# Optimization experiments

Measured on AMD Instinct MI355X. Metric: run time of the kernel, lower is better.

Reference implementation:

```python
import jax, jax.numpy as jnp
import numpy as np

B, S, V, E, H, NL, DFF = 16, 16, 64, 64, 8, 4, 2048
L = S * V
DH = E // H
NUM_GRIDS = 100
POI_DIM = 8
OV_DIM = 8


def setup_inputs() -> dict:
    key = jax.random.key(0)
    ks = jax.random.split(key, 32)
    sc = 0.05
    inp = {}
    inp['features'] = jax.random.normal(ks[0], (B, S, V, 3), jnp.float32)
    inp['overlap_tag'] = jax.random.randint(ks[1], (B, S, V), 0, 3)
    inp['poi_id'] = jax.random.randint(ks[2], (B, S, V), 0, NUM_GRIDS + 1)
    # embedders
    inp['W_raw'] = jax.random.normal(ks[3], (3, E), jnp.float32) * sc
    inp['b_raw'] = jnp.zeros((E,), jnp.float32)
    inp['pos_tab'] = jax.random.normal(ks[4], (S, E), jnp.float32) * sc
    inp['type_tab'] = jax.random.normal(ks[5], (V, E), jnp.float32) * sc
    inp['poi_tab'] = jax.random.normal(ks[6], (NUM_GRIDS + 1, POI_DIM), jnp.float32) * sc
    inp['overlap_tab'] = jax.random.normal(ks[7], (3, OV_DIM), jnp.float32) * sc
    inp['W_comb'] = jax.random.normal(ks[8], (E + OV_DIM + POI_DIM, E), jnp.float32) * sc
    inp['b_comb'] = jnp.zeros((E,), jnp.float32)
    # transformer layers (stacked over NL)
    inp['Wqkv'] = jax.random.normal(ks[9], (NL, E, 3 * E), jnp.float32) * sc
    inp['bqkv'] = jnp.zeros((NL, 3 * E), jnp.float32)
    inp['Wo'] = jax.random.normal(ks[10], (NL, E, E), jnp.float32) * sc
    inp['bo'] = jnp.zeros((NL, E), jnp.float32)
    inp['ln1_s'] = jnp.ones((NL, E), jnp.float32)
    inp['ln1_b'] = jnp.zeros((NL, E), jnp.float32)
    inp['W1'] = jax.random.normal(ks[11], (NL, E, DFF), jnp.float32) * sc
    inp['b1'] = jnp.zeros((NL, DFF), jnp.float32)
    inp['W2'] = jax.random.normal(ks[12], (NL, DFF, E), jnp.float32) * sc
    inp['b2'] = jnp.zeros((NL, E), jnp.float32)
    inp['ln2_s'] = jnp.ones((NL, E), jnp.float32)
    inp['ln2_b'] = jnp.zeros((NL, E), jnp.float32)
    inp['W_head'] = jax.random.normal(ks[13], (E, 3), jnp.float32) * sc
    inp['b_head'] = jnp.zeros((3,), jnp.float32)
    return inp


def _layer_norm(x, s, b):
    m = x.mean(-1, keepdims=True)
    v = ((x - m) ** 2).mean(-1, keepdims=True)
    return (x - m) / jnp.sqrt(v + 1e-5) * s + b


def _forward(features, overlap_tag, poi_id, W_raw, b_raw, pos_tab, type_tab,
             poi_tab, overlap_tab, W_comb, b_comb, Wqkv, bqkv, Wo, bo,
             ln1_s, ln1_b, W1, b1, W2, b2, ln2_s, ln2_b, W_head, b_head):
    # padding_idx=0 rows are zero (as in nn.Embedding(padding_idx=0))
    poi_tab = poi_tab.at[0].set(0.0)
    overlap_tab = overlap_tab.at[0].set(0.0)

    zero_mask = (features.sum(-1) == 0).reshape(B, L)  # [B, L]
    ov_idx = jnp.maximum(overlap_tag, 0)
    poi_idx = jnp.maximum(poi_id, 0)

    feat_e = features @ W_raw + b_raw                    # [B,S,V,E]
    concat = jnp.concatenate([feat_e, overlap_tab[ov_idx], poi_tab[poi_idx]], axis=-1)
    x = (concat @ W_comb + b_comb).reshape(B, L, E)      # [B,L,E]

    t_idx = jnp.repeat(jnp.arange(S), V)                 # [L]
    v_idx = jnp.tile(jnp.arange(V), S)                   # [L]
    struct_mask = (t_idx[:, None] != t_idx[None, :]) & (v_idx[:, None] != v_idx[None, :])
    full_mask = struct_mask[None] | zero_mask[:, None, :] | zero_mask[:, :, None]  # [B,L,L]
    bias = jnp.where(full_mask, -jnp.inf, 0.0)[:, None, :, :]  # [B,1,L,L]

    x = x + pos_tab[t_idx][None] + type_tab[v_idx][None]

    scale = 1.0 / jnp.sqrt(jnp.asarray(DH, x.dtype))
    for l in range(NL):
        qkv = x @ Wqkv[l] + bqkv[l]                      # [B,L,3E]
        q, k, v = jnp.split(qkv, 3, axis=-1)
        q = q.reshape(B, L, H, DH)
        k = k.reshape(B, L, H, DH)
        v = v.reshape(B, L, H, DH)
        scores = jnp.einsum('bqhd,bkhd->bhqk', q, k) * scale + bias
        attn = jax.nn.softmax(scores, axis=-1)
        o = jnp.einsum('bhqk,bkhd->bqhd', attn, v).reshape(B, L, E)
        x = _layer_norm(x + o @ Wo[l] + bo[l], ln1_s[l], ln1_b[l])
        ff = jax.nn.relu(x @ W1[l] + b1[l]) @ W2[l] + b2[l]
        x = _layer_norm(x + ff, ln2_s[l], ln2_b[l])

    last = x.reshape(B, S, V, E)[:, -1]                  # [B,V,E]
    return last @ W_head + b_head                        # [B,V,3]


def reference(features, overlap_tag, poi_id, W_raw, b_raw, pos_tab, type_tab,
              poi_tab, overlap_tab, W_comb, b_comb, Wqkv, bqkv, Wo, bo,
              ln1_s, ln1_b, W1, b1, W2, b2, ln2_s, ln2_b, W_head, b_head):
    return _forward(features, overlap_tag, poi_id, W_raw, b_raw, pos_tab, type_tab,
                    poi_tab, overlap_tab, W_comb, b_comb, Wqkv, bqkv, Wo, bo,
                    ln1_s, ln1_b, W1, b1, W2, b2, ln2_s, ln2_b, W_head, b_head)
```

## Files before the change

kernel.cpp:

```cpp
#include <hip/hip_runtime.h>
#include <math.h>

#define BB 16
#define SS 16
#define VVV 64
#define EE 64
#define HHH 8
#define NLAYER 4
#define DFF_ 2048
#define LL 1024
#define BL 16384
#define PERL 131072

typedef __attribute__((ext_vector_type(8))) _Float16 half8;
typedef __attribute__((ext_vector_type(4))) _Float16 half4v;
typedef __attribute__((ext_vector_type(2))) _Float16 half2v;
typedef __attribute__((ext_vector_type(4))) float f32x4;

#if defined(__has_builtin)
#if __has_builtin(__builtin_amdgcn_fdot2)
#define HAVE_FDOT2 1
#endif
#endif

#define SW64(m, k)  (((m) << 6) + ((((k) >> 3) ^ ((m) & 7)) << 3) + ((k) & 7))


__global__ __launch_bounds__(256) void k_prep(
    const float* __restrict__ W1, const float* __restrict__ W2,
    const float* __restrict__ Wqkv, const float* __restrict__ Wo,
    const float* __restrict__ Wcomb,
    _Float16* __restrict__ w1f, _Float16* __restrict__ w2f,
    _Float16* __restrict__ wqkvf, _Float16* __restrict__ wof,
    _Float16* __restrict__ wcombt)
{
  __shared__ float t[64 * 65];
  int bx = blockIdx.x;
  int cc = threadIdx.x & 63, rr = threadIdx.x >> 6;

  if (bx >= 272) {
    int r0 = (bx - 272) * 64;
#pragma unroll
    for (int i = 0; i < 16; i++) {
      int r = i * 4 + rr;
      if (r0 + r < 80) t[r * 65 + cc] = Wcomb[(size_t)(r0 + r) * 64 + cc];
    }
    __syncthreads();
#pragma unroll
    for (int i = 0; i < 16; i++) {
      int c = i * 4 + rr;
      if (r0 + c < 80) wcombt[(size_t)cc * 80 + r0 + c] = (_Float16)t[c * 65 + cc];
    }
    return;
  }

  const float* src; _Float16* dst; int astr;
  if (bx < 128) {
    int l = bx >> 5, g = bx & 31;
    src = W1 + (size_t)l * PERL + g * 64; astr = 2048;
    dst = w1f + (size_t)(l * 32 + g) * 4096;
  } else if (bx < 256) {
    int j = bx - 128; int l = j >> 5, g = j & 31;
    src = W2 + (size_t)l * PERL + (size_t)g * 64 * 64; astr = 64;
    dst = w2f + (size_t)(l * 32 + g) * 4096;
  } else if (bx < 268) {
    int j = bx - 256; int l = j / 3, g = j % 3;
    src = Wqkv + (size_t)l * 64 * 192 + g * 64; astr = 192;
    dst = wqkvf + (size_t)(l * 3 + g) * 4096;
  } else {
    int l = bx - 268;
    src = Wo + (size_t)l * 4096; astr = 64;
    dst = wof + (size_t)l * 4096;
  }
#pragma unroll
  for (int i = 0; i < 16; i++) {
    int a = i * 4 + rr;
    t[cc * 65 + a] = src[(size_t)a * astr + cc];
  }
  __syncthreads();
#pragma unroll
  for (int it = 0; it < 2; it++) {
    int c = threadIdx.x + it * 256;
    int frag = c >> 6, lane = c & 63;
    int m = (frag >> 1) * 16 + (lane & 15);
    int k0 = (frag & 1) * 32 + (lane >> 4) * 8;
    const float* tr = &t[m * 65 + k0];
    half8 h;
#pragma unroll
    for (int j = 0; j < 8; j++) h[j] = (_Float16)tr[j];
    *(half8*)&dst[(size_t)c * 8] = h;
  }
}

__device__ __forceinline__ void qkv_nb(
    const half8 (&af)[2][2], const _Float16* __restrict__ wqkvf,
    const float* __restrict__ bqkv, _Float16* __restrict__ qbuf,
    _Float16* __restrict__ kbuf, _Float16* __restrict__ vbuf,
    int bx, int nb, int wm, int wn, int lane)
{
  int quad = lane >> 4, l15 = lane & 15;
  const _Float16* bt = wqkvf + (size_t)nb * 4096;
  half8 bf[2][2];
#pragma unroll
  for (int nt = 0; nt < 2; nt++)
#pragma unroll
    for (int ks = 0; ks < 2; ks++)
      bf[nt][ks] = *(const half8*)&bt[(size_t)(((wn * 2 + nt) * 2 + ks) * 512) +
                                      lane * 8];
  f32x4 acc[2][2];
#pragma unroll
  for (int mt = 0; mt < 2; mt++)
#pragma unroll
    for (int nt = 0; nt < 2; nt++) {
      float bv = bqkv[nb * 64 + wn * 32 + nt * 16 + l15];
      acc[mt][nt] = (f32x4){bv, bv, bv, bv};
    }
#pragma unroll
  for (int ks = 0; ks < 2; ks++)
#pragma unroll
    for (int mt = 0; mt < 2; mt++)
#pragma unroll
      for (int nt = 0; nt < 2; nt++)
        acc[mt][nt] = __builtin_amdgcn_mfma_f32_16x16x32_f16(
            af[mt][ks], bf[nt][ks], acc[mt][nt], 0, 0, 0);
  _Float16* dst = (nb == 0) ? qbuf : ((nb == 1) ? kbuf : vbuf);
#pragma unroll
  for (int mt = 0; mt < 2; mt++)
#pragma unroll
    for (int nt = 0; nt < 2; nt++) {
      int col = wn * 32 + nt * 16 + l15;
      int h = col >> 3, d = col & 7;
#pragma unroll
      for (int r = 0; r < 4; r++) {
        int row = bx * 64 + wm * 32 + mt * 16 + quad * 4 + r;
        int b = row >> 10, rb = row & 1023;
        dst[((size_t)(b * 8 + h) * 1024 + rb) * 8 + d] = (_Float16)acc[mt][nt][r];
      }
    }
}

__global__ __launch_bounds__(256) void k_embqkv(
    const float* __restrict__ features, const int* __restrict__ ovtag,
    const int* __restrict__ poiid, const float* __restrict__ W_raw,
    const float* __restrict__ b_raw, const float* __restrict__ ov_tab,
    const float* __restrict__ poi_tab, const _Float16* __restrict__ wcombt,
    const float* __restrict__ b_comb, const float* __restrict__ pos_tab,
    const float* __restrict__ type_tab, float* __restrict__ x1,
    float* __restrict__ zm, const _Float16* __restrict__ wqkvf,
    const float* __restrict__ bqkv, _Float16* __restrict__ qbuf,
    _Float16* __restrict__ kbuf, _Float16* __restrict__ vbuf)
{
  constexpr int KP = 104;
  __shared__ _Float16 As[64 * KP];
  __shared__ _Float16 Bs[64 * KP];
  __shared__ _Float16 xs[4096];
  int tid = threadIdx.x;
  int raw = blockIdx.x;
  int bx = ((raw & 7) * 2 + ((raw >> 3) >> 4)) * 16 + ((raw >> 3) & 15);
  int m0 = bx * 64;
  int wave = tid >> 6, lane = tid & 63, quad = lane >> 4, l15 = lane & 15;
  int wm = wave >> 1, wn = wave & 1;
  for (int p = tid; p < 1536; p += 256) {
    int r = p / 24, s = p - r * 24; int c = s * 4;
    int row = m0 + r;
    float f0 = features[row * 3 + 0];
    float f1 = features[row * 3 + 1];
    float f2 = features[row * 3 + 2];
    if (s == 0) zm[row] = ((f0 + f1 + f2) == 0.f) ? 1.f : 0.f;
    half4v h;
#pragma unroll
    for (int j = 0; j < 4; j++) {
      int cc = c + j; float v;
      if (cc < 64) {
        v = b_raw[cc] + f0 * W_raw[cc] + f1 * W_raw[64 + cc] + f2 * W_raw[128 + cc];
      } else if (cc < 72) {
        int tt = ovtag[row]; v = (tt <= 0) ? 0.f : ov_tab[tt * 8 + cc - 64];
      } else if (cc < 80) {
        int tt = poiid[row]; v = (tt <= 0) ? 0.f : poi_tab[tt * 8 + cc - 72];
      } else v = 0.f;
      h[j] = (_Float16)v;
    }
    *(half4v*)&As[r * KP + c] = h;
  }
  for (int p = tid; p < 1536; p += 256) {
    int r = p / 24, s = p - r * 24; int c = s * 4;
    half4v h = (half4v){0, 0, 0, 0};
    if (c < 80) h = *(const half4v*)&wcombt[r * 80 + c];
    *(half4v*)&Bs[r * KP + c] = h;
  }
  __syncthreads();
  f32x4 acc[2][2];
#pragma unroll
  for (int mt = 0; mt < 2; mt++)
#pragma unroll
    for (int nt = 0; nt < 2; nt++) {
      float bv = b_comb[wn * 32 + nt * 16 + l15];
      acc[mt][nt] = (f32x4){bv, bv, bv, bv};
    }
#pragma unroll
  for (int ks = 0; ks < 3; ks++) {
    half8 af[2], bf[2];
#pragma unroll
    for (int mt = 0; mt < 2; mt++)
      af[mt] = *(const half8*)&As[(wm * 32 + mt * 16 + l15) * KP + ks * 32 + quad * 8];
#pragma unroll
    for (int nt = 0; nt < 2; nt++)
      bf[nt] = *(const half8*)&Bs[(wn * 32 + nt * 16 + l15) * KP + ks * 32 + quad * 8];
#pragma unroll
    for (int mt = 0; mt < 2; mt++)
#pragma unroll
      for (int nt = 0; nt < 2; nt++)
        acc[mt][nt] = __builtin_amdgcn_mfma_f32_16x16x32_f16(af[mt], bf[nt],
                                                             acc[mt][nt], 0, 0, 0);
  }
#pragma unroll
  for (int mt = 0; mt < 2; mt++)
#pragma unroll
    for (int nt = 0; nt < 2; nt++)
#pragma unroll
      for (int r = 0; r < 4; r++) {
        int lrow = wm * 32 + mt * 16 + quad * 4 + r;
        int row = m0 + lrow;
        int col = wn * 32 + nt * 16 + l15;
        int l = row & (LL - 1);
        float v = acc[mt][nt][r] +
            pos_tab[(l >> 6) * 64 + col] + type_tab[(l & 63) * 64 + col];
        x1[(size_t)row * 64 + col] = v;
        xs[SW64(lrow, col)] = (_Float16)v;
      }
  __syncthreads();
  half8 af[2][2];
#pragma unroll
  for (int mt = 0; mt < 2; mt++)
#pragma unroll
    for (int ks = 0; ks < 2; ks++)
      af[mt][ks] = *(const half8*)&xs[SW64(wm * 32 + mt * 16 + l15,
                                           ks * 32 + quad * 8)];
  for (int nb = 0; nb < 3; nb++)
    qkv_nb(af, wqkvf, bqkv, qbuf, kbuf, vbuf, bx, nb, wm, wn, lane);
}

__global__ __launch_bounds__(256, 4) void k_layer16(
    const _Float16* __restrict__ qin, const _Float16* __restrict__ kin,
    const _Float16* __restrict__ vin, const float* __restrict__ zm,
    const _Float16* __restrict__ wof, const float* __restrict__ bo,
    float* __restrict__ x1,
    const float* __restrict__ ln1_s, const float* __restrict__ ln1_b,
    const _Float16* __restrict__ w1f, const _Float16* __restrict__ w2f,
    const float* __restrict__ b1, const float* __restrict__ b2,
    const float* __restrict__ ln2_s, const float* __restrict__ ln2_b,
    const _Float16* __restrict__ wqkvf, const float* __restrict__ bqkv,
    _Float16* __restrict__ qout, _Float16* __restrict__ kout,
    _Float16* __restrict__ vout, int doqkv,
    const float* __restrict__ Wh, const float* __restrict__ bh,
    float* __restrict__ out)
{
  __shared__ float ots[16 * 68];
  __shared__ float ots2[16 * 68];
  __shared__ __align__(16) _Float16 xs[1024];
  __shared__ float x2f[1024];
  __shared__ __align__(16) _Float16 hs[4][1024];
  __shared__ __align__(16) _Float16 os[1024];
  __shared__ float zsh[1024];
  __shared__ __align__(16) _Float16 qkvt[16 * 200];
  int tid = threadIdx.x;
  int raw = blockIdx.x;
  int bx = ((raw & 7) * 2 + ((raw >> 3) >> 6)) * 64 + ((raw >> 3) & 63);
  int r0 = bx * 16;
  int rb0 = r0 & 1023;
  int b = r0 >> 10;
  int wave = tid >> 6, lane = tid & 63;
  int quad = lane >> 4, l15 = lane & 15;

  for (int p = tid; p < 1024; p += 256)
    zsh[p] = (zm[b * LL + p] != 0.f) ? -20000.f : 0.f;

  half8 obf[2];
#pragma unroll
  for (int ks = 0; ks < 2; ks++)
    obf[ks] = *(const half8*)&wof[(size_t)((wave * 2 + ks) * 512) + lane * 8];
  float x1pre[4];
#pragma unroll
  for (int i = 0; i < 4; i++)
    x1pre[i] = x1[(size_t)(r0 + wave * 4 + i) * 64 + lane];
  float ln1sv = ln1_s[lane], ln1bv = ln1_b[lane];
  float ln2sv = ln2_s[lane], ln2bv = ln2_b[lane];
  float fb2 = b2[lane];
  float bov = bo[wave * 16 + l15];
  __syncthreads();

  {
    int pr = tid >> 1, ksl = tid & 1;
    int lr = pr & 15, hh = pr >> 4;
    int rb = rb0 + lr;
    int tq = rb0 >> 6;
    int vq = rb & 63;
    const _Float16* kb = kin + (size_t)(b * 8 + hh) * 8192;
    const _Float16* vb = vin + (size_t)(b * 8 + hh) * 8192;
    half8 qh = *(const half8*)&qin[(size_t)(b * 8 + hh) * 8192 + (size_t)rb * 8];
    const float scale = 0.3535533905932738f;
    float m = -10000.f, lsum = 0.f;
    float acc[8] = {0.f, 0.f, 0.f, 0.f, 0.f, 0.f, 0.f, 0.f};
    bool zmq = (zsh[rb] < -1.f);

    auto attend = [&](int k) {
      half8 kk = *(const half8*)&kb[(size_t)k * 8];
      half8 vv = *(const half8*)&vb[(size_t)k * 8];
      float s = 0.f;
#ifdef HAVE_FDOT2
#pragma unroll
      for (int j = 0; j < 4; j++) {
        half2v qa = (half2v){qh[2 * j], qh[2 * j + 1]};
        half2v ka = (half2v){kk[2 * j], kk[2 * j + 1]};
        s = __builtin_amdgcn_fdot2(qa, ka, s, false);
      }
#else
#pragma unroll
      for (int j = 0; j < 8; j++) s += (float)qh[j] * (float)kk[j];
#endif
      s = s * scale + zsh[k];
      float nm = fmaxf(m, s);
      float r = __expf(m - nm);
      float p = __expf(s - nm);
      lsum = lsum * r + p;
#pragma unroll
      for (int d = 0; d < 8; d++) acc[d] = acc[d] * r + p * (float)vv[d];
      m = nm;
    };

    if (!zmq) {
#pragma unroll 4
      for (int i = 0; i < 32; i++) attend(tq * 64 + 2 * i + ksl);
      int c = 0;
      for (int tt = 0; tt < 16; tt++) {
        if (tt == tq) continue;
        if ((c & 1) == ksl) attend(tt * 64 + vq);
        c++;
      }
    }
    float m2 = __shfl_xor(m, 1), l2 = __shfl_xor(lsum, 1);
    float nm = fmaxf(m, m2);
    float f1 = __expf(m - nm), f2 = __expf(m2 - nm);
    lsum = lsum * f1 + l2 * f2;
#pragma unroll
    for (int d = 0; d < 8; d++) {
      float a2 = __shfl_xor(acc[d], 1);
      acc[d] = acc[d] * f1 + a2 * f2;
    }
    float inv = (lsum > 0.f) ? 1.f / lsum : 0.f;
    if (ksl == 0) {
      half8 o;
#pragma unroll
      for (int d = 0; d < 8; d++) o[d] = (_Float16)(acc[d] * inv);
      *(half8*)&os[SW64(lr, hh * 8)] = o;
    }
  }
  __syncthreads();

  {
    half8 af[2];
#pragma unroll
    for (int ks = 0; ks < 2; ks++)
      af[ks] = *(const half8*)&os[SW64(l15, ks * 32 + quad * 8)];
    f32x4 acc = (f32x4){bov, bov, bov, bov};
#pragma unroll
    for (int ks = 0; ks < 2; ks++)
      acc = __builtin_amdgcn_mfma_f32_16x16x32_f16(af[ks], obf[ks], acc, 0, 0, 0);
#pragma unroll
    for (int r = 0; r < 4; r++)
      ots[(quad * 4 + r) * 68 + wave * 16 + l15] = acc[r];
  }
  __syncthreads();
  for (int i = 0; i < 4; i++) {
    int row = wave * 4 + i;
    float val = ots[row * 68 + lane] + x1pre[i];
    float sum = val;
#pragma unroll
    for (int o = 32; o > 0; o >>= 1) sum += __shfl_xor(sum, o);
    float mean = sum * (1.f / 64.f);
    float d = val - mean;
    float sq = d * d;
#pragma unroll
    for (int o = 32; o > 0; o >>= 1) sq += __shfl_xor(sq, o);
    float xv = d * rsqrtf(sq * (1.f / 64.f) + 1e-5f) * ln1sv + ln1bv;
    x2f[row * 64 + lane] = xv;
    xs[SW64(row, lane)] = (_Float16)xv;
  }
  __syncthreads();

  half8 xb[2];
#pragma unroll
  for (int ks = 0; ks < 2; ks++)
    xb[ks] = *(const half8*)&xs[SW64(l15, ks * 32 + quad * 8)];
  f32x4 facc[4];
#pragma unroll
  for (int nt = 0; nt < 4; nt++) facc[nt] = (f32x4){0.f, 0.f, 0.f, 0.f};
  _Float16* hw = &hs[wave][0];
  for (int ii = 0; ii < 8; ii++) {
    int g = ii * 4 + wave;
    const _Float16* w1t = w1f + (size_t)g * 4096;
    const _Float16* w2t = w2f + (size_t)g * 4096;
    half8 a1[4][2], b2w[4][2];
#pragma unroll
    for (int t = 0; t < 4; t++)
#pragma unroll
      for (int ks = 0; ks < 2; ks++) {
        a1[t][ks] = *(const half8*)&w1t[(size_t)((t * 2 + ks) * 512) + lane * 8];
        b2w[t][ks] = *(const half8*)&w2t[(size_t)((t * 2 + ks) * 512) + lane * 8];
      }
    f32x4 hacc[4];
#pragma unroll
    for (int ht = 0; ht < 4; ht++) hacc[ht] = (f32x4){0.f, 0.f, 0.f, 0.f};
#pragma unroll
    for (int ks = 0; ks < 2; ks++)
#pragma unroll
      for (int ht = 0; ht < 4; ht++)
        hacc[ht] = __builtin_amdgcn_mfma_f32_16x16x32_f16(a1[ht][ks], xb[ks],
                                                          hacc[ht], 0, 0, 0);
#pragma unroll
    for (int ht = 0; ht < 4; ht++) {
      float4 bb = *(const float4*)&b1[g * 64 + ht * 16 + quad * 4];
      f32x4 hv = hacc[ht];
      half4v hp = (half4v){
          (_Float16)fmaxf(hv[0] + bb.x, 0.f), (_Float16)fmaxf(hv[1] + bb.y, 0.f),
          (_Float16)fmaxf(hv[2] + bb.z, 0.f), (_Float16)fmaxf(hv[3] + bb.w, 0.f)};
      *(half4v*)&hw[SW64(l15, ht * 16 + quad * 4)] = hp;
    }
#pragma unroll
    for (int ks = 0; ks < 2; ks++) {
      half8 a2 = *(const half8*)&hw[SW64(l15, ks * 32 + quad * 8)];
#pragma unroll
      for (int nt = 0; nt < 4; nt++)
        facc[nt] = __builtin_amdgcn_mfma_f32_16x16x32_f16(a2, b2w[nt][ks],
                                                          facc[nt], 0, 0, 0);
    }
  }
  if (wave < 2) {
    float* dst = (wave == 0) ? ots : ots2;
#pragma unroll
    for (int nt = 0; nt < 4; nt++)
#pragma unroll
      for (int r = 0; r < 4; r++)
        dst[(quad * 4 + r) * 68 + nt * 16 + l15] = facc[nt][r];
  }
  __syncthreads();
  if (wave >= 2) {
    float* dst = (wave == 2) ? ots : ots2;
#pragma unroll
    for (int nt = 0; nt < 4; nt++)
#pragma unroll
      for (int r = 0; r < 4; r++)
        dst[(quad * 4 + r) * 68 + nt * 16 + l15] += facc[nt][r];
  }
  __syncthreads();
  for (int i = 0; i < 4; i++) {
    int row = wave * 4 + i;
    size_t off = (size_t)(r0 + row) * 64 + lane;
    float val = ots[row * 68 + lane] + ots2[row * 68 + lane] + fb2 +
                x2f[row * 64 + lane];
    float sum = val;
#pragma unroll
    for (int o = 32; o > 0; o >>= 1) sum += __shfl_xor(sum, o);
    float mean = sum * (1.f / 64.f);
    float d = val - mean;
    float sq = d * d;
#pragma unroll
    for (int o = 32; o > 0; o >>= 1) sq += __shfl_xor(sq, o);
    float xv = d * rsqrtf(sq * (1.f / 64.f) + 1e-5f) * ln2sv + ln2bv;
    x1[off] = xv;
    x2f[row * 64 + lane] = xv;
    xs[SW64(row, lane)] = (_Float16)xv;
  }
  __syncthreads();
  if (!doqkv) {
    if ((bx & 63) >= 60 && tid < 48) {
      int bb2 = bx >> 6;
      int i = tid / 3, j = tid - i * 3;
      int vglob = (bx & 3) * 16 + i;
      float a = bh[j];
      for (int e = 0; e < 64; e++)
        a += x2f[i * 64 + e] * Wh[e * 3 + j];
      out[((size_t)(bb2 * 64 + vglob)) * 3 + j] = a;
    }
    return;
  }
  {
    half8 af[2];
#pragma unroll
    for (int ks = 0; ks < 2; ks++)
      af[ks] = *(const half8*)&xs[SW64(l15, ks * 32 + quad * 8)];
#pragma unroll
    for (int nb = 0; nb < 3; nb++) {
      const _Float16* bt = wqkvf + (size_t)nb * 4096;
      half8 bf[2];
#pragma unroll
      for (int ks = 0; ks < 2; ks++)
        bf[ks] = *(const half8*)&bt[(size_t)((wave * 2 + ks) * 512) + lane * 8];
      float bv = bqkv[nb * 64 + wave * 16 + l15];
      f32x4 qacc = (f32x4){bv, bv, bv, bv};
#pragma unroll
      for (int ks = 0; ks < 2; ks++)
        qacc = __builtin_amdgcn_mfma_f32_16x16x32_f16(af[ks], bf[ks], qacc,
                                                      0, 0, 0);
#pragma unroll
      for (int r = 0; r < 4; r++)
        qkvt[(quad * 4 + r) * 200 + nb * 64 + wave * 16 + l15] = (_Float16)qacc[r];
    }
  }
  __syncthreads();
  for (int p = tid; p < 384; p += 256) {
    int buf = p >> 7;
    int idx = p & 127;
    int h = idx >> 4, lr = idx & 15;
    _Float16* dst = (buf == 0) ? qout : ((buf == 1) ? kout : vout);
    half8 v = *(const half8*)&qkvt[lr * 200 + buf * 64 + h * 8];
    *(half8*)&dst[((size_t)(b * 8 + h) * 1024 + rb0 + lr) * 8] = v;
  }
}

extern "C" void kernel_launch(void* const* d_in, const int* in_sizes, int n_in,
                              void* d_out, int out_size, void* d_ws, size_t ws_size,
                              hipStream_t stream) {
  const float* features = (const float*)d_in[0];
  const int*   ovtag    = (const int*)d_in[1];
  const int*   poiid    = (const int*)d_in[2];
  const float* W_raw    = (const float*)d_in[3];
  const float* b_raw    = (const float*)d_in[4];
  const float* pos_tab  = (const float*)d_in[5];
  const float* type_tab = (const float*)d_in[6];
  const float* poi_tab  = (const float*)d_in[7];
  const float* ov_tab   = (const float*)d_in[8];
  const float* W_comb   = (const float*)d_in[9];
  const float* b_comb   = (const float*)d_in[10];
  const float* Wqkv     = (const float*)d_in[11];
  const float* bqkv     = (const float*)d_in[12];
  const float* Wo       = (const float*)d_in[13];
  const float* bo       = (const float*)d_in[14];
  const float* ln1_s    = (const float*)d_in[15];
  const float* ln1_b    = (const float*)d_in[16];
  const float* W1       = (const float*)d_in[17];
  const float* b1       = (const float*)d_in[18];
  const float* W2       = (const float*)d_in[19];
  const float* b2       = (const float*)d_in[20];
  const float* ln2_s    = (const float*)d_in[21];
  const float* ln2_b    = (const float*)d_in[22];
  const float* W_head   = (const float*)d_in[23];
  const float* b_head   = (const float*)d_in[24];
  float* out = (float*)d_out;
  float* ws  = (float*)d_ws;

  float* zm  = ws;
  float* x1  = zm + BL;
  _Float16* qbA = (_Float16*)(x1 + (size_t)BL * 64);
  _Float16* kbA = qbA + (size_t)BL * 64;
  _Float16* vbA = kbA + (size_t)BL * 64;
  _Float16* qbB = vbA + (size_t)BL * 64;
  _Float16* kbB = qbB + (size_t)BL * 64;
  _Float16* vbB = kbB + (size_t)BL * 64;
  _Float16* wcombt = vbB + (size_t)BL * 64;
  _Float16* w1f    = wcombt + 5120;
  _Float16* w2f    = w1f + (size_t)NLAYER * PERL;
  _Float16* wqkvf  = w2f + (size_t)NLAYER * PERL;
  _Float16* wof    = wqkvf + (size_t)NLAYER * 3 * 4096;

  k_prep<<<274, 256, 0, stream>>>(W1, W2, Wqkv, Wo, W_comb,
                                  w1f, w2f, wqkvf, wof, wcombt);
  k_embqkv<<<256, 256, 0, stream>>>(features, ovtag, poiid, W_raw, b_raw,
                                    ov_tab, poi_tab, wcombt, b_comb,
                                    pos_tab, type_tab, x1, zm,
                                    wqkvf, bqkv, qbA, kbA, vbA);
  for (int l = 0; l < NLAYER; l++) {
    const _Float16* qin = (l & 1) ? qbB : qbA;
    const _Float16* kin = (l & 1) ? kbB : kbA;
    const _Float16* vin = (l & 1) ? vbB : vbA;
    _Float16* qout = (l & 1) ? qbA : qbB;
    _Float16* kout = (l & 1) ? kbA : kbB;
    _Float16* vout = (l & 1) ? vbA : vbB;
    int doqkv = (l < NLAYER - 1);
    k_layer16<<<1024, 256, 0, stream>>>(
        qin, kin, vin, zm,
        wof + (size_t)l * 4096, bo + l * EE, x1,
        ln1_s + l * EE, ln1_b + l * EE,
        w1f + (size_t)l * PERL, w2f + (size_t)l * PERL,
        b1 + l * DFF_, b2 + l * EE,
        ln2_s + l * EE, ln2_b + l * EE,
        wqkvf + (size_t)(l + 1 < NLAYER ? l + 1 : 0) * 3 * 4096,
        bqkv + (l + 1 < NLAYER ? l + 1 : 0) * 192,
        qout, kout, vout, doqkv, W_head, b_head, out);
  }
}
```

Measured before the change: 312.5 us.

## Stage QKV stores through LDS, batch attention loads, and cut register pressure in FFN

In the embedding kernel, QKV results are now staged in shared memory and written out as coalesced 16-byte vectors, replacing scattered 2-byte global stores. The attention inner loop batches four K/V loads ahead of the dot products and uses a branchy online-softmax update that skips one exp when the max does not change. The FFN loop reuses one register array for the W1 and W2 fragments, lowering register pressure. The layer kernel's qkvt buffer now aliases the hs scratch to save LDS, and the block-index swizzles are simplified. The trade-off is more LDS use and an extra sync in the embed kernel, plus divergent branches in the softmax update.

```diff
diff --git a/kernel.cpp b/kernel.cpp
--- a/kernel.cpp
+++ b/kernel.cpp
@@ -92,53 +92,6 @@
   }
 }
 
-__device__ __forceinline__ void qkv_nb(
-    const half8 (&af)[2][2], const _Float16* __restrict__ wqkvf,
-    const float* __restrict__ bqkv, _Float16* __restrict__ qbuf,
-    _Float16* __restrict__ kbuf, _Float16* __restrict__ vbuf,
-    int bx, int nb, int wm, int wn, int lane)
-{
-  int quad = lane >> 4, l15 = lane & 15;
-  const _Float16* bt = wqkvf + (size_t)nb * 4096;
-  half8 bf[2][2];
-#pragma unroll
-  for (int nt = 0; nt < 2; nt++)
-#pragma unroll
-    for (int ks = 0; ks < 2; ks++)
-      bf[nt][ks] = *(const half8*)&bt[(size_t)(((wn * 2 + nt) * 2 + ks) * 512) +
-                                      lane * 8];
-  f32x4 acc[2][2];
-#pragma unroll
-  for (int mt = 0; mt < 2; mt++)
-#pragma unroll
-    for (int nt = 0; nt < 2; nt++) {
-      float bv = bqkv[nb * 64 + wn * 32 + nt * 16 + l15];
-      acc[mt][nt] = (f32x4){bv, bv, bv, bv};
-    }
-#pragma unroll
-  for (int ks = 0; ks < 2; ks++)
-#pragma unroll
-    for (int mt = 0; mt < 2; mt++)
-#pragma unroll
-      for (int nt = 0; nt < 2; nt++)
-        acc[mt][nt] = __builtin_amdgcn_mfma_f32_16x16x32_f16(
-            af[mt][ks], bf[nt][ks], acc[mt][nt], 0, 0, 0);
-  _Float16* dst = (nb == 0) ? qbuf : ((nb == 1) ? kbuf : vbuf);
-#pragma unroll
-  for (int mt = 0; mt < 2; mt++)
-#pragma unroll
-    for (int nt = 0; nt < 2; nt++) {
-      int col = wn * 32 + nt * 16 + l15;
-      int h = col >> 3, d = col & 7;
-#pragma unroll
-      for (int r = 0; r < 4; r++) {
-        int row = bx * 64 + wm * 32 + mt * 16 + quad * 4 + r;
-        int b = row >> 10, rb = row & 1023;
-        dst[((size_t)(b * 8 + h) * 1024 + rb) * 8 + d] = (_Float16)acc[mt][nt][r];
-      }
-    }
-}
-
 __global__ __launch_bounds__(256) void k_embqkv(
     const float* __restrict__ features, const int* __restrict__ ovtag,
     const int* __restrict__ poiid, const float* __restrict__ W_raw,
@@ -151,12 +104,13 @@
     _Float16* __restrict__ kbuf, _Float16* __restrict__ vbuf)
 {
   constexpr int KP = 104;
-  __shared__ _Float16 As[64 * KP];
-  __shared__ _Float16 Bs[64 * KP];
-  __shared__ _Float16 xs[4096];
+  __shared__ __align__(16) _Float16 As[64 * KP];
+  __shared__ __align__(16) _Float16 Bs[64 * KP];
+  __shared__ __align__(16) _Float16 xs[4096];
+  __shared__ __align__(16) _Float16 qkvt[64 * 200];
   int tid = threadIdx.x;
   int raw = blockIdx.x;
-  int bx = ((raw & 7) * 2 + ((raw >> 3) >> 4)) * 16 + ((raw >> 3) & 15);
+  int bx = ((raw & 7) << 5) + (raw >> 3);
   int m0 = bx * 64;
   int wave = tid >> 6, lane = tid & 63, quad = lane >> 4, l15 = lane & 15;
   int wm = wave >> 1, wn = wave & 1;
@@ -236,8 +190,49 @@
     for (int ks = 0; ks < 2; ks++)
       af[mt][ks] = *(const half8*)&xs[SW64(wm * 32 + mt * 16 + l15,
                                            ks * 32 + quad * 8)];
-  for (int nb = 0; nb < 3; nb++)
-    qkv_nb(af, wqkvf, bqkv, qbuf, kbuf, vbuf, bx, nb, wm, wn, lane);
+#pragma unroll
+  for (int nb = 0; nb < 3; nb++) {
+    const _Float16* bt = wqkvf + (size_t)nb * 4096;
+    half8 bf[2][2];
+#pragma unroll
+    for (int nt = 0; nt < 2; nt++)
+#pragma unroll
+      for (int ks = 0; ks < 2; ks++)
+        bf[nt][ks] = *(const half8*)&bt[(size_t)(((wn * 2 + nt) * 2 + ks) * 512) +
+                                        lane * 8];
+    f32x4 qacc[2][2];
+#pragma unroll
+    for (int mt = 0; mt < 2; mt++)
+#pragma unroll
+      for (int nt = 0; nt < 2; nt++) {
+        float bv = bqkv[nb * 64 + wn * 32 + nt * 16 + l15];
+        qacc[mt][nt] = (f32x4){bv, bv, bv, bv};
+      }
+#pragma unroll
+    for (int ks = 0; ks < 2; ks++)
+#pragma unroll
+      for (int mt = 0; mt < 2; mt++)
+#pragma unroll
+        for (int nt = 0; nt < 2; nt++)
+          qacc[mt][nt] = __builtin_amdgcn_mfma_f32_16x16x32_f16(
+              af[mt][ks], bf[nt][ks], qacc[mt][nt], 0, 0, 0);
+#pragma unroll
+    for (int mt = 0; mt < 2; mt++)
+#pragma unroll
+      for (int nt = 0; nt < 2; nt++)
+#pragma unroll
+        for (int r = 0; r < 4; r++)
+          qkvt[(wm * 32 + mt * 16 + quad * 4 + r) * 200 + nb * 64 +
+               wn * 32 + nt * 16 + l15] = (_Float16)qacc[mt][nt][r];
+  }
+  __syncthreads();
+  int bq = m0 >> 10, rq0 = m0 & 1023;
+  for (int p = tid; p < 1536; p += 256) {
+    int buf = p >> 9, rem = p & 511, h = rem >> 6, row = rem & 63;
+    _Float16* dst = (buf == 0) ? qbuf : ((buf == 1) ? kbuf : vbuf);
+    half8 v = *(const half8*)&qkvt[row * 200 + buf * 64 + h * 8];
+    *(half8*)&dst[((size_t)(bq * 8 + h) * 1024 + rq0 + row) * 8] = v;
+  }
 }
 
 __global__ __launch_bounds__(256, 4) void k_layer16(
@@ -262,10 +257,9 @@
   __shared__ __align__(16) _Float16 hs[4][1024];
   __shared__ __align__(16) _Float16 os[1024];
   __shared__ float zsh[1024];
-  __shared__ __align__(16) _Float16 qkvt[16 * 200];
   int tid = threadIdx.x;
   int raw = blockIdx.x;
-  int bx = ((raw & 7) * 2 + ((raw >> 3) >> 6)) * 64 + ((raw >> 3) & 63);
+  int bx = ((raw & 7) << 7) + (raw >> 3);
   int r0 = bx * 16;
   int rb0 = r0 & 1023;
   int b = r0 >> 10;
@@ -303,9 +297,7 @@
     float acc[8] = {0.f, 0.f, 0.f, 0.f, 0.f, 0.f, 0.f, 0.f};
     bool zmq = (zsh[rb] < -1.f);
 
-    auto attend = [&](int k) {
-      half8 kk = *(const half8*)&kb[(size_t)k * 8];
-      half8 vv = *(const half8*)&vb[(size_t)k * 8];
+    auto dot = [&](half8 kk) -> float {
       float s = 0.f;
 #ifdef HAVE_FDOT2
 #pragma unroll
@@ -318,24 +310,61 @@
 #pragma unroll
       for (int j = 0; j < 8; j++) s += (float)qh[j] * (float)kk[j];
 #endif
-      s = s * scale + zsh[k];
-      float nm = fmaxf(m, s);
-      float r = __expf(m - nm);
-      float p = __expf(s - nm);
-      lsum = lsum * r + p;
-#pragma unroll
-      for (int d = 0; d < 8; d++) acc[d] = acc[d] * r + p * (float)vv[d];
-      m = nm;
+      return s;
     };
+    auto update = [&](float s, half8 vv) {
+      if (s > m) {
+        float r = __expf(m - s);
+        lsum = lsum * r + 1.f;
+#pragma unroll
+        for (int d = 0; d < 8; d++) acc[d] = acc[d] * r + (float)vv[d];
+        m = s;
+      } else {
+        float p = __expf(s - m);
+        lsum += p;
+#pragma unroll
+        for (int d = 0; d < 8; d++) acc[d] += p * (float)vv[d];
+      }
+    };
 
     if (!zmq) {
-#pragma unroll 4
-      for (int i = 0; i < 32; i++) attend(tq * 64 + 2 * i + ksl);
-      int c = 0;
-      for (int tt = 0; tt < 16; tt++) {
-        if (tt == tq) continue;
-        if ((c & 1) == ksl) attend(tt * 64 + vq);
-        c++;
+      for (int base = 0; base < 32; base += 4) {
+        half8 kk[4], vv[4]; float sv[4];
+#pragma unroll
+        for (int j = 0; j < 4; j++) {
+          int k = tq * 64 + 2 * (base + j) + ksl;
+          kk[j] = *(const half8*)&kb[(size_t)k * 8];
+          vv[j] = *(const half8*)&vb[(size_t)k * 8];
+          sv[j] = zsh[k];
+        }
+#pragma unroll
+        for (int j = 0; j < 4; j++) sv[j] += dot(kk[j]) * scale;
+#pragma unroll
+        for (int j = 0; j < 4; j++) update(sv[j], vv[j]);
+      }
+      for (int bb2 = 0; bb2 < 2; bb2++) {
+        half8 kk[4], vv[4]; float sv[4];
+#pragma unroll
+        for (int j = 0; j < 4; j++) {
+          int cc = 2 * (bb2 * 4 + j) + ksl;
+          if (cc < 15) {
+            int tt = cc + ((cc >= tq) ? 1 : 0);
+            int k = tt * 64 + vq;
+            kk[j] = *(const half8*)&kb[(size_t)k * 8];
+            vv[j] = *(const half8*)&vb[(size_t)k * 8];
+            sv[j] = zsh[k];
+          }
+        }
+#pragma unroll
+        for (int j = 0; j < 4; j++) {
+          int cc = 2 * (bb2 * 4 + j) + ksl;
+          if (cc < 15) sv[j] += dot(kk[j]) * scale;
+        }
+#pragma unroll
+        for (int j = 0; j < 4; j++) {
+          int cc = 2 * (bb2 * 4 + j) + ksl;
+          if (cc < 15) update(sv[j], vv[j]);
+        }
       }
     }
     float m2 = __shfl_xor(m, 1), l2 = __shfl_xor(lsum, 1);
@@ -398,16 +427,13 @@
   _Float16* hw = &hs[wave][0];
   for (int ii = 0; ii < 8; ii++) {
     int g = ii * 4 + wave;
+    half8 w[4][2];
     const _Float16* w1t = w1f + (size_t)g * 4096;
-    const _Float16* w2t = w2f + (size_t)g * 4096;
-    half8 a1[4][2], b2w[4][2];
 #pragma unroll
     for (int t = 0; t < 4; t++)
 #pragma unroll
-      for (int ks = 0; ks < 2; ks++) {
-        a1[t][ks] = *(const half8*)&w1t[(size_t)((t * 2 + ks) * 512) + lane * 8];
-        b2w[t][ks] = *(const half8*)&w2t[(size_t)((t * 2 + ks) * 512) + lane * 8];
-      }
+      for (int ks = 0; ks < 2; ks++)
+        w[t][ks] = *(const half8*)&w1t[(size_t)((t * 2 + ks) * 512) + lane * 8];
     f32x4 hacc[4];
 #pragma unroll
     for (int ht = 0; ht < 4; ht++) hacc[ht] = (f32x4){0.f, 0.f, 0.f, 0.f};
@@ -415,7 +441,7 @@
     for (int ks = 0; ks < 2; ks++)
 #pragma unroll
       for (int ht = 0; ht < 4; ht++)
-        hacc[ht] = __builtin_amdgcn_mfma_f32_16x16x32_f16(a1[ht][ks], xb[ks],
+        hacc[ht] = __builtin_amdgcn_mfma_f32_16x16x32_f16(w[ht][ks], xb[ks],
                                                           hacc[ht], 0, 0, 0);
 #pragma unroll
     for (int ht = 0; ht < 4; ht++) {
@@ -426,12 +452,18 @@
           (_Float16)fmaxf(hv[2] + bb.z, 0.f), (_Float16)fmaxf(hv[3] + bb.w, 0.f)};
       *(half4v*)&hw[SW64(l15, ht * 16 + quad * 4)] = hp;
     }
+    const _Float16* w2t = w2f + (size_t)g * 4096;
+#pragma unroll
+    for (int t = 0; t < 4; t++)
+#pragma unroll
+      for (int ks = 0; ks < 2; ks++)
+        w[t][ks] = *(const half8*)&w2t[(size_t)((t * 2 + ks) * 512) + lane * 8];
 #pragma unroll
     for (int ks = 0; ks < 2; ks++) {
       half8 a2 = *(const half8*)&hw[SW64(l15, ks * 32 + quad * 8)];
 #pragma unroll
       for (int nt = 0; nt < 4; nt++)
-        facc[nt] = __builtin_amdgcn_mfma_f32_16x16x32_f16(a2, b2w[nt][ks],
+        facc[nt] = __builtin_amdgcn_mfma_f32_16x16x32_f16(a2, w[nt][ks],
                                                           facc[nt], 0, 0, 0);
     }
   }
@@ -484,6 +516,7 @@
     }
     return;
   }
+  _Float16* qkvt = &hs[0][0];
   {
     half8 af[2];
 #pragma unroll
@@ -509,12 +542,10 @@
   }
   __syncthreads();
   for (int p = tid; p < 384; p += 256) {
-    int buf = p >> 7;
-    int idx = p & 127;
-    int h = idx >> 4, lr = idx & 15;
+    int buf = p >> 7, rem = p & 127, h = rem >> 4, row = rem & 15;
     _Float16* dst = (buf == 0) ? qout : ((buf == 1) ? kout : vout);
-    half8 v = *(const half8*)&qkvt[lr * 200 + buf * 64 + h * 8];
-    *(half8*)&dst[((size_t)(b * 8 + h) * 1024 + rb0 + lr) * 8] = v;
+    half8 v = *(const half8*)&qkvt[row * 200 + buf * 64 + h * 8];
+    *(half8*)&dst[((size_t)(b * 8 + h) * 1024 + rb0 + row) * 8] = v;
   }
 }
 
```

After: 287.6 us. 8.0% less time.
